# Kernel tuning notes

Hardware: AMD Instinct MI355X
Metric: run time of the kernel (lower is better)

Reference implementation:

```python
import jax, jax.numpy as jnp
import numpy as np

EMB = 1024

def setup_inputs() -> dict:
    key = jax.random.key(0)
    ks = jax.random.split(key, 6)
    B, S, E = 4, 2048, EMB
    x = jax.random.normal(ks[0], (B, S, E), dtype=jnp.float32)
    attention_mask = jax.random.randint(ks[1], (B, S, S), 0, 2, dtype=jnp.int32)
    proj_w = jax.random.normal(ks[2], (E, 3 * E), dtype=jnp.float32) * (1.0 / np.sqrt(E))
    proj_b = jax.random.normal(ks[3], (3 * E,), dtype=jnp.float32) * 0.02
    out_w = jax.random.normal(ks[4], (E, E), dtype=jnp.float32) * (1.0 / np.sqrt(E))
    out_b = jax.random.normal(ks[5], (E,), dtype=jnp.float32) * 0.02
    return {"x": x, "attention_mask": attention_mask, "proj_w": proj_w,
            "proj_b": proj_b, "out_w": out_w, "out_b": out_b}

def reference(x, attention_mask, proj_w, proj_b, out_w, out_b):
    E = x.shape[-1]
    scale = 1.0 / jnp.sqrt(jnp.asarray(E, x.dtype))
    qkv = x @ proj_w + proj_b                      # [B,S,3E]
    q, k, v = jnp.split(qkv, 3, axis=-1)           # each [B,S,E]
    scores = jnp.einsum('bqe,bke->bqk', q, k) * scale  # [B,S,S]
    scores = jnp.where(attention_mask == 0, jnp.asarray(-1e20, scores.dtype), scores)
    attn = jax.nn.softmax(scores, axis=-1)
    ctx = jnp.einsum('bqk,bke->bqe', attn, v)      # [B,S,E]
    return ctx @ out_w + out_b
```

## Files before the change

kernel.cpp:

```cpp
#include <hip/hip_runtime.h>
#include <cstdint>

typedef unsigned short u16;
typedef __bf16 bf16x8 __attribute__((ext_vector_type(8)));
typedef float f32x4 __attribute__((ext_vector_type(4)));

__device__ __forceinline__ u16 f2bf(float f) {
  unsigned u = __float_as_uint(f);
  u += 0x7fffu + ((u >> 16) & 1u);
  return (u16)(u >> 16);
}

__device__ __forceinline__ void async16(const void* g, void* l) {
  __builtin_amdgcn_global_load_lds(
      (const __attribute__((address_space(1))) uint32_t*)g,
      (__attribute__((address_space(3))) uint32_t*)l, 16, 0, 0);
}

__global__ void k_cvt(const float* __restrict__ in, u16* __restrict__ out, int n4) {
  int i = blockIdx.x * blockDim.x + threadIdx.x;
  if (i >= n4) return;
  const float4 v = ((const float4*)in)[i];
  ushort4 o;
  o.x = f2bf(v.x); o.y = f2bf(v.y); o.z = f2bf(v.z); o.w = f2bf(v.w);
  ((ushort4*)out)[i] = o;
}

__device__ __forceinline__ u16 to_bf(float v) { return f2bf(v); }
__device__ __forceinline__ u16 to_bf(u16 v) { return v; }

template <typename Tin>
__global__ void k_transpose(const Tin* __restrict__ in, u16* __restrict__ out,
                            int lda, int ldo, long bsIn, long bsOut) {
  __shared__ u16 tile[32][33];
  const int b = blockIdx.z;
  in += (size_t)b * bsIn;
  out += (size_t)b * bsOut;
  const int c0 = blockIdx.x * 32, r0 = blockIdx.y * 32;
  const int tx = threadIdx.x, ty = threadIdx.y;
#pragma unroll
  for (int i = 0; i < 4; ++i) {
    int r = r0 + ty + i * 8;
    tile[ty + i * 8][tx] = to_bf(in[(size_t)r * lda + c0 + tx]);
  }
  __syncthreads();
#pragma unroll
  for (int i = 0; i < 4; ++i) {
    out[(size_t)(c0 + ty + i * 8) * ldo + r0 + tx] = tile[tx][ty + i * 8];
  }
}

__global__ __launch_bounds__(256) void k_maskexp(u16* __restrict__ SP,
                                                 const int* __restrict__ mask,
                                                 float* __restrict__ lsum) {
  const int w = threadIdx.x >> 6, lane = threadIdx.x & 63;
  const int row = blockIdx.x * 4 + w;
  const size_t base = (size_t)row * 2048;
  float s = 0.f;
#pragma unroll
  for (int c = 0; c < 4; ++c) {
    const size_t idx = base + c * 512 + lane * 8;
    bf16x8 v = *(const bf16x8*)(SP + idx);
    const int4 m0 = *(const int4*)(mask + idx);
    const int4 m1 = *(const int4*)(mask + idx + 4);
    float e[8];
    const int mk[8] = {m0.x, m0.y, m0.z, m0.w, m1.x, m1.y, m1.z, m1.w};
#pragma unroll
    for (int j = 0; j < 8; ++j) {
      float f = __expf(fminf((float)v[j], 80.f));
      e[j] = mk[j] ? f : 0.f;
      s += e[j];
      v[j] = (__bf16)e[j];
    }
    *(bf16x8*)(SP + idx) = v;
  }
#pragma unroll
  for (int off = 32; off > 0; off >>= 1) s += __shfl_down(s, off, 64);
  if (lane == 0) lsum[row] = s;
}

template <int MODE>
__global__ __launch_bounds__(256) void gemm_bt(
    const u16* __restrict__ A, long lda, long bsA,
    const u16* __restrict__ Bt, long ldb, long bsB,
    void* __restrict__ C, long ldc, long bsC,
    int M, int N, int K,
    const float* __restrict__ bias, const float* __restrict__ lsum) {
  __shared__ u16 As[128 * 64];
  __shared__ u16 Bs[128 * 64];

  const int b = blockIdx.z;
  const int m0 = blockIdx.y * 128, n0 = blockIdx.x * 128;
  const int lane = threadIdx.x & 63;
  const int w = threadIdx.x >> 6;
  const int wr = w >> 1, wc = w & 1;

  const int srow = lane >> 3;
  const int scol = ((lane & 7) ^ (lane >> 3 & 7)) * 8;
  const u16* pa = A + (size_t)b * bsA + (size_t)(m0 + srow) * lda + scol;
  const u16* pb = Bt + (size_t)b * bsB + (size_t)(n0 + srow) * ldb + scol;

  const int m_l = lane & 15, q = lane >> 4, m7 = m_l & 7;
  const int offs[2] = {(q ^ m7) * 8, ((4 + q) ^ m7) * 8};

  f32x4 acc[4][4] = {};

  for (int kt = 0; kt < K; kt += 64) {
    __syncthreads();
#pragma unroll
    for (int g = 0; g < 4; ++g) {
      const int c = w * 4 + g;
      async16(pa + (size_t)(c * 8) * lda, As + c * 512);
      async16(pb + (size_t)(c * 8) * ldb, Bs + c * 512);
    }
    __syncthreads();
#pragma unroll
    for (int s = 0; s < 2; ++s) {
      bf16x8 af[4], bfr[4];
#pragma unroll
      for (int t = 0; t < 4; ++t)
        af[t] = *(const bf16x8*)(As + (wr * 64 + t * 16 + m_l) * 64 + offs[s]);
#pragma unroll
      for (int t = 0; t < 4; ++t)
        bfr[t] = *(const bf16x8*)(Bs + (wc * 64 + t * 16 + m_l) * 64 + offs[s]);
#pragma unroll
      for (int mt = 0; mt < 4; ++mt)
#pragma unroll
        for (int nt = 0; nt < 4; ++nt)
          acc[mt][nt] = __builtin_amdgcn_mfma_f32_16x16x32_bf16(af[mt], bfr[nt], acc[mt][nt], 0, 0, 0);
    }
    pa += 64;
    pb += 64;
  }

#pragma unroll
  for (int mt = 0; mt < 4; ++mt) {
#pragma unroll
    for (int nt = 0; nt < 4; ++nt) {
      const int col = n0 + wc * 64 + nt * 16 + (lane & 15);
      const int row0 = m0 + wr * 64 + mt * 16 + ((lane >> 4) << 2);
#pragma unroll
      for (int r = 0; r < 4; ++r) {
        const int row = row0 + r;
        float v = acc[mt][nt][r];
        if constexpr (MODE == 0) {
          v += bias[col];
          if (col < 1024) v *= 0.03125f;
          ((u16*)C)[(size_t)b * bsC + (size_t)row * ldc + col] = f2bf(v);
        } else if constexpr (MODE == 1) {
          ((u16*)C)[(size_t)b * bsC + (size_t)row * ldc + col] = f2bf(v);
        } else if constexpr (MODE == 2) {
          v = v / lsum[(size_t)b * M + row];
          ((u16*)C)[(size_t)b * bsC + (size_t)row * ldc + col] = f2bf(v);
        } else {
          v += bias[col];
          ((float*)C)[(size_t)b * bsC + (size_t)row * ldc + col] = v;
        }
      }
    }
  }
}

extern "C" void kernel_launch(void* const* d_in, const int* in_sizes, int n_in,
                              void* d_out, int out_size, void* d_ws, size_t ws_size,
                              hipStream_t stream) {
  const float* x = (const float*)d_in[0];
  const int* mask = (const int*)d_in[1];
  const float* proj_w = (const float*)d_in[2];
  const float* proj_b = (const float*)d_in[3];
  const float* out_w = (const float*)d_in[4];
  const float* out_b = (const float*)d_in[5];
  float* out = (float*)d_out;

  char* ws = (char*)d_ws;
  u16* xb = (u16*)(ws);
  u16* wt = (u16*)(ws + 16777216);
  u16* owt = (u16*)(ws + 23068672);
  u16* qkv = (u16*)(ws + 25165824);
  u16* P = (u16*)(ws + 75497472);
  u16* Vt = (u16*)(ws + 109051904);
  float* lsum = (float*)(ws + 125829120);
  u16* ctx = xb;

  k_cvt<<<8192, 256, 0, stream>>>(x, xb, 2097152);
  k_transpose<float><<<dim3(96, 32, 1), dim3(32, 8), 0, stream>>>(proj_w, wt, 3072, 1024, 0, 0);
  k_transpose<float><<<dim3(32, 32, 1), dim3(32, 8), 0, stream>>>(out_w, owt, 1024, 1024, 0, 0);
  gemm_bt<0><<<dim3(24, 64, 1), 256, 0, stream>>>(xb, 1024, 0, wt, 1024, 0, qkv, 3072, 0,
                                                  8192, 3072, 1024, proj_b, nullptr);
  k_transpose<u16><<<dim3(32, 64, 4), dim3(32, 8), 0, stream>>>(
      qkv + 2048, Vt, 3072, 2048, (long)2048 * 3072, (long)1024 * 2048);
  gemm_bt<1><<<dim3(16, 16, 4), 256, 0, stream>>>(
      qkv, 3072, (long)2048 * 3072, qkv + 1024, 3072, (long)2048 * 3072,
      P, 2048, (long)2048 * 2048, 2048, 2048, 1024, nullptr, nullptr);
  k_maskexp<<<2048, 256, 0, stream>>>(P, mask, lsum);
  gemm_bt<2><<<dim3(8, 16, 4), 256, 0, stream>>>(
      P, 2048, (long)2048 * 2048, Vt, 2048, (long)1024 * 2048,
      ctx, 1024, (long)2048 * 1024, 2048, 1024, 2048, nullptr, lsum);
  gemm_bt<3><<<dim3(8, 64, 1), 256, 0, stream>>>(ctx, 1024, 0, owt, 1024, 0, out, 1024, 0,
                                                 8192, 1024, 1024, out_b, nullptr);
}
```

Measured before the change: 350.3 us.

## Fuse mask and exp into QK GEMM epilogue via bitpacked mask, MFMA row sums

```diff
diff --git a/kernel.cpp b/kernel.cpp
--- a/kernel.cpp
+++ b/kernel.cpp
@@ -2,6 +2,7 @@
 #include <cstdint>
 
 typedef unsigned short u16;
+typedef uint32_t u32;
 typedef __bf16 bf16x8 __attribute__((ext_vector_type(8)));
 typedef float f32x4 __attribute__((ext_vector_type(4)));
 
@@ -50,33 +51,20 @@
   }
 }
 
-__global__ __launch_bounds__(256) void k_maskexp(u16* __restrict__ SP,
-                                                 const int* __restrict__ mask,
-                                                 float* __restrict__ lsum) {
-  const int w = threadIdx.x >> 6, lane = threadIdx.x & 63;
-  const int row = blockIdx.x * 4 + w;
-  const size_t base = (size_t)row * 2048;
-  float s = 0.f;
-#pragma unroll
-  for (int c = 0; c < 4; ++c) {
-    const size_t idx = base + c * 512 + lane * 8;
-    bf16x8 v = *(const bf16x8*)(SP + idx);
-    const int4 m0 = *(const int4*)(mask + idx);
-    const int4 m1 = *(const int4*)(mask + idx + 4);
-    float e[8];
-    const int mk[8] = {m0.x, m0.y, m0.z, m0.w, m1.x, m1.y, m1.z, m1.w};
-#pragma unroll
-    for (int j = 0; j < 8; ++j) {
-      float f = __expf(fminf((float)v[j], 80.f));
-      e[j] = mk[j] ? f : 0.f;
-      s += e[j];
-      v[j] = (__bf16)e[j];
-    }
-    *(bf16x8*)(SP + idx) = v;
-  }
-#pragma unroll
-  for (int off = 32; off > 0; off >>= 1) s += __shfl_down(s, off, 64);
-  if (lane == 0) lsum[row] = s;
+__global__ __launch_bounds__(256) void k_bitpack(const int* __restrict__ mask,
+                                                 u32* __restrict__ mbits) {
+  const size_t w = (size_t)blockIdx.x * 256 + threadIdx.x;
+  const int* p = mask + w * 32;
+  u32 bits = 0;
+#pragma unroll
+  for (int j = 0; j < 8; ++j) {
+    const int4 v = ((const int4*)p)[j];
+    bits |= (u32)(v.x & 1) << (j * 4 + 0);
+    bits |= (u32)(v.y & 1) << (j * 4 + 1);
+    bits |= (u32)(v.z & 1) << (j * 4 + 2);
+    bits |= (u32)(v.w & 1) << (j * 4 + 3);
+  }
+  mbits[w] = bits;
 }
 
 template <int MODE>
@@ -85,7 +73,7 @@
     const u16* __restrict__ Bt, long ldb, long bsB,
     void* __restrict__ C, long ldc, long bsC,
     int M, int N, int K,
-    const float* __restrict__ bias, const float* __restrict__ lsum) {
+    const float* __restrict__ bias, const u32* __restrict__ mbits) {
   __shared__ u16 As[128 * 64];
   __shared__ u16 Bs[128 * 64];
 
@@ -96,7 +84,7 @@
   const int wr = w >> 1, wc = w & 1;
 
   const int srow = lane >> 3;
-  const int scol = ((lane & 7) ^ (lane >> 3 & 7)) * 8;
+  const int scol = ((lane & 7) ^ ((lane >> 3) & 7)) * 8;
   const u16* pa = A + (size_t)b * bsA + (size_t)(m0 + srow) * lda + scol;
   const u16* pb = Bt + (size_t)b * bsB + (size_t)(n0 + srow) * ldb + scol;
 
@@ -104,6 +92,10 @@
   const int offs[2] = {(q ^ m7) * 8, ((4 + q) ^ m7) * 8};
 
   f32x4 acc[4][4] = {};
+  f32x4 accs[4] = {};
+  bf16x8 ones;
+#pragma unroll
+  for (int e = 0; e < 8; ++e) ones[e] = (__bf16)1.0f;
 
   for (int kt = 0; kt < K; kt += 64) {
     __syncthreads();
@@ -128,17 +120,39 @@
 #pragma unroll
         for (int nt = 0; nt < 4; ++nt)
           acc[mt][nt] = __builtin_amdgcn_mfma_f32_16x16x32_bf16(af[mt], bfr[nt], acc[mt][nt], 0, 0, 0);
+      if constexpr (MODE == 2) {
+#pragma unroll
+        for (int mt = 0; mt < 4; ++mt)
+          accs[mt] = __builtin_amdgcn_mfma_f32_16x16x32_bf16(af[mt], ones, accs[mt], 0, 0, 0);
+      }
     }
     pa += 64;
     pb += 64;
   }
 
+  if constexpr (MODE == 1) {
+    __syncthreads();
+    const int rl = threadIdx.x >> 1, pr = threadIdx.x & 1;
+    const uint2 v = *(const uint2*)(mbits + ((size_t)(b * M + m0 + rl)) * (N >> 5) + (n0 >> 5) + pr * 2);
+    ((u32*)As)[rl * 4 + pr * 2] = v.x;
+    ((u32*)As)[rl * 4 + pr * 2 + 1] = v.y;
+    __syncthreads();
+  }
+
+  float rinv[4][4];
+  if constexpr (MODE == 2) {
+#pragma unroll
+    for (int mt = 0; mt < 4; ++mt)
+#pragma unroll
+      for (int r = 0; r < 4; ++r) rinv[mt][r] = 1.0f / accs[mt][r];
+  }
+
 #pragma unroll
   for (int mt = 0; mt < 4; ++mt) {
 #pragma unroll
     for (int nt = 0; nt < 4; ++nt) {
-      const int col = n0 + wc * 64 + nt * 16 + (lane & 15);
-      const int row0 = m0 + wr * 64 + mt * 16 + ((lane >> 4) << 2);
+      const int col = n0 + wc * 64 + nt * 16 + m_l;
+      const int row0 = m0 + wr * 64 + mt * 16 + q * 4;
 #pragma unroll
       for (int r = 0; r < 4; ++r) {
         const int row = row0 + r;
@@ -148,9 +162,13 @@
           if (col < 1024) v *= 0.03125f;
           ((u16*)C)[(size_t)b * bsC + (size_t)row * ldc + col] = f2bf(v);
         } else if constexpr (MODE == 1) {
+          const int cl = wc * 64 + nt * 16 + m_l;
+          const int rl = wr * 64 + mt * 16 + q * 4 + r;
+          const u32 wb = ((const u32*)As)[rl * 4 + (cl >> 5)];
+          v = ((wb >> (cl & 31)) & 1u) ? __expf(fminf(v, 30.f)) : 0.f;
           ((u16*)C)[(size_t)b * bsC + (size_t)row * ldc + col] = f2bf(v);
         } else if constexpr (MODE == 2) {
-          v = v / lsum[(size_t)b * M + row];
+          v *= rinv[mt][r];
           ((u16*)C)[(size_t)b * bsC + (size_t)row * ldc + col] = f2bf(v);
         } else {
           v += bias[col];
@@ -179,23 +197,23 @@
   u16* qkv = (u16*)(ws + 25165824);
   u16* P = (u16*)(ws + 75497472);
   u16* Vt = (u16*)(ws + 109051904);
-  float* lsum = (float*)(ws + 125829120);
   u16* ctx = xb;
+  u32* mbits = (u32*)wt;
 
   k_cvt<<<8192, 256, 0, stream>>>(x, xb, 2097152);
   k_transpose<float><<<dim3(96, 32, 1), dim3(32, 8), 0, stream>>>(proj_w, wt, 3072, 1024, 0, 0);
   k_transpose<float><<<dim3(32, 32, 1), dim3(32, 8), 0, stream>>>(out_w, owt, 1024, 1024, 0, 0);
   gemm_bt<0><<<dim3(24, 64, 1), 256, 0, stream>>>(xb, 1024, 0, wt, 1024, 0, qkv, 3072, 0,
                                                   8192, 3072, 1024, proj_b, nullptr);
+  k_bitpack<<<2048, 256, 0, stream>>>(mask, mbits);
   k_transpose<u16><<<dim3(32, 64, 4), dim3(32, 8), 0, stream>>>(
       qkv + 2048, Vt, 3072, 2048, (long)2048 * 3072, (long)1024 * 2048);
   gemm_bt<1><<<dim3(16, 16, 4), 256, 0, stream>>>(
       qkv, 3072, (long)2048 * 3072, qkv + 1024, 3072, (long)2048 * 3072,
-      P, 2048, (long)2048 * 2048, 2048, 2048, 1024, nullptr, nullptr);
-  k_maskexp<<<2048, 256, 0, stream>>>(P, mask, lsum);
+      P, 2048, (long)2048 * 2048, 2048, 2048, 1024, nullptr, mbits);
   gemm_bt<2><<<dim3(8, 16, 4), 256, 0, stream>>>(
       P, 2048, (long)2048 * 2048, Vt, 2048, (long)1024 * 2048,
-      ctx, 1024, (long)2048 * 1024, 2048, 1024, 2048, nullptr, lsum);
+      ctx, 1024, (long)2048 * 1024, 2048, 1024, 2048, nullptr, nullptr);
   gemm_bt<3><<<dim3(8, 64, 1), 256, 0, stream>>>(ctx, 1024, 0, owt, 1024, 0, out, 1024, 0,
                                                  8192, 1024, 1024, out_b, nullptr);
 }
```

New measurement: 349.4 us. No clear change (-0.2%).
